# Performance work log

Hardware: AMD Instinct MI355X
Metric: run time of the kernel (lower is better)

The kernel has to match this reference:

```python
import jax, jax.numpy as jnp
import numpy as np

N_HEAD, D_MODEL, D_K, D_V, D_O = 16, 1024, 64, 64, 1024
B, S = 4, 2048


def setup_inputs() -> dict:
    key = jax.random.key(0)
    ks = jax.random.split(key, 11)
    s = 0.02
    return {
        "q": jax.random.normal(ks[0], (B, S, D_MODEL), jnp.float32),
        "k": jax.random.normal(ks[1], (B, S, D_MODEL), jnp.float32),
        "v": jax.random.normal(ks[2], (B, S, D_MODEL), jnp.float32),
        "Wq": jax.random.normal(ks[3], (D_MODEL, N_HEAD * D_K), jnp.float32) * s,
        "bq": jnp.zeros((N_HEAD * D_K,), jnp.float32),
        "Wk": jax.random.normal(ks[4], (D_MODEL, N_HEAD * D_K), jnp.float32) * s,
        "bk": jnp.zeros((N_HEAD * D_K,), jnp.float32),
        "Wv": jax.random.normal(ks[5], (D_MODEL, N_HEAD * D_V), jnp.float32) * s,
        "bv": jnp.zeros((N_HEAD * D_V,), jnp.float32),
        "Wo": jax.random.normal(ks[6], (N_HEAD * D_V, D_O), jnp.float32) * s,
        "bo": jnp.zeros((D_O,), jnp.float32),
    }


def reference(q, k, v, Wq, bq, Wk, bk, Wv, bv, Wo, bo):
    b, n_q, _ = q.shape
    # QKV projections -> [b, s, h, d]
    qh = (q @ Wq + bq).reshape(b, -1, N_HEAD, D_K)
    kh = (k @ Wk + bk).reshape(b, -1, N_HEAD, D_K)
    vh = (v @ Wv + bv).reshape(b, -1, N_HEAD, D_V)
    scale = jnp.asarray(np.power(D_K, 0.5), qh.dtype)
    # scores [b, h, n_q, n_k]
    scores = jnp.einsum("bqhd,bkhd->bhqk", qh, kh) / scale
    attn = jax.nn.softmax(scores, axis=-1)
    out = jnp.einsum("bhqk,bkhd->bqhd", attn, vh).reshape(b, n_q, N_HEAD * D_V)
    return out @ Wo + bo
```

## Files before the change

### kernel.cpp

```cpp
#include <hip/hip_runtime.h>
#include <hip/hip_bf16.h>


typedef __attribute__((ext_vector_type(8))) short bf16x8;
typedef __attribute__((ext_vector_type(4))) float f32x4;
typedef __attribute__((ext_vector_type(4))) unsigned short u16x4;

#define QSCALE 0.1803368801111244f

__device__ __forceinline__ unsigned short f2bf(float x) {
  unsigned u = __builtin_bit_cast(unsigned, x);
  u += 0x7fffu + ((u >> 16) & 1u);
  return (unsigned short)(u >> 16);
}

__device__ __forceinline__ short f2bf_s(float x) {
  __hip_bfloat16 h = __float2bfloat16(x);
  return __builtin_bit_cast(short, h);
}

__device__ __forceinline__ float fexp2(float x) {
#if __has_builtin(__builtin_amdgcn_exp2f)
  return __builtin_amdgcn_exp2f(x);
#else
  return exp2f(x);
#endif
}

__global__ void wtrans4(const float* __restrict__ W0, const float* __restrict__ W1,
                        const float* __restrict__ W2, const float* __restrict__ W3,
                        unsigned short* __restrict__ WT) {
  __shared__ float t[32][33];
  int x = threadIdx.x, y = threadIdx.y;
  int k0 = blockIdx.x * 32, n0 = blockIdx.y * 32;
  int z = blockIdx.z;
  const float* W = z == 0 ? W0 : z == 1 ? W1 : z == 2 ? W2 : W3;
  float scale = z == 0 ? QSCALE : 1.0f;
  unsigned short* dst = WT + (size_t)z * (1024 * 1024);
#pragma unroll
  for (int i = 0; i < 4; i++)
    t[y + i * 8][x] = W[(k0 + y + i * 8) * 1024 + n0 + x];
  __syncthreads();
#pragma unroll
  for (int i = 0; i < 4; i++)
    dst[(n0 + y + i * 8) * 1024 + k0 + x] = f2bf(t[x][y + i * 8] * scale);
}

template <bool AF32, int MODE>
__global__ __launch_bounds__(256, 2) void gemm128(
    const void* __restrict__ Ap, const unsigned short* __restrict__ BT,
    const float* __restrict__ bias, float bscale, void* __restrict__ Cp) {
  __shared__ __align__(16) char As[8192];
  __shared__ __align__(16) char Bs[8192];
  const int K = 1024;
  int tid = threadIdx.x;
  int lane = tid & 63;
  int w = tid >> 6;
  int wr = w >> 1, wc = w & 1;
  int bid = blockIdx.x;
  int sid = (bid & 7) * 64 + (bid >> 3);
  int m0 = (sid >> 3) * 128, n0 = (sid & 7) * 128;
  int r = tid >> 1;
  int kb = (tid & 1) << 4;

  f32x4 acc[4][4];
#pragma unroll
  for (int i = 0; i < 4; i++)
#pragma unroll
    for (int j = 0; j < 4; j++) acc[i][j] = (f32x4){0.f, 0.f, 0.f, 0.f};

  const float* Af = (const float*)Ap;
  const unsigned short* Ab = (const unsigned short*)Ap;

  f32x4 afr[4];
  bf16x8 afb[2];
  bf16x8 bfr[2];

  if (AF32) {
    const f32x4* p = (const f32x4*)(Af + (size_t)(m0 + r) * K + kb);
#pragma unroll
    for (int i = 0; i < 4; i++) afr[i] = p[i];
  } else {
    const bf16x8* p = (const bf16x8*)(Ab + (size_t)(m0 + r) * K + kb);
    afb[0] = p[0]; afb[1] = p[1];
  }
  {
    const bf16x8* p = (const bf16x8*)(BT + (size_t)(n0 + r) * K + kb);
    bfr[0] = p[0]; bfr[1] = p[1];
  }

  int swz = (r & 7) << 4;
  int wbyte = r * 64 + kb * 2;
  int cc = lane & 15, g = lane >> 4;

  for (int k0 = 0; k0 < K; k0 += 32) {
    __syncthreads();
    if (AF32) {
      bf16x8 s0, s1;
#pragma unroll
      for (int i = 0; i < 8; i++) {
        s0[i] = (short)f2bf(afr[i >> 2][i & 3]);
        s1[i] = (short)f2bf(afr[2 + (i >> 2)][i & 3]);
      }
      *(bf16x8*)(As + (wbyte ^ swz)) = s0;
      *(bf16x8*)(As + ((wbyte + 16) ^ swz)) = s1;
    } else {
      *(bf16x8*)(As + (wbyte ^ swz)) = afb[0];
      *(bf16x8*)(As + ((wbyte + 16) ^ swz)) = afb[1];
    }
    *(bf16x8*)(Bs + (wbyte ^ swz)) = bfr[0];
    *(bf16x8*)(Bs + ((wbyte + 16) ^ swz)) = bfr[1];
    if (k0 + 32 < K) {
      if (AF32) {
        const f32x4* p = (const f32x4*)(Af + (size_t)(m0 + r) * K + k0 + 32 + kb);
#pragma unroll
        for (int i = 0; i < 4; i++) afr[i] = p[i];
      } else {
        const bf16x8* p = (const bf16x8*)(Ab + (size_t)(m0 + r) * K + k0 + 32 + kb);
        afb[0] = p[0]; afb[1] = p[1];
      }
      const bf16x8* p = (const bf16x8*)(BT + (size_t)(n0 + r) * K + k0 + 32 + kb);
      bfr[0] = p[0]; bfr[1] = p[1];
    }
    __syncthreads();
    bf16x8 a[4], b[4];
#pragma unroll
    for (int mi = 0; mi < 4; mi++) {
      int row = wr * 64 + mi * 16 + cc;
      int byte = (row * 64 + g * 16) ^ ((row & 7) << 4);
      a[mi] = *(const bf16x8*)(As + byte);
    }
#pragma unroll
    for (int ni = 0; ni < 4; ni++) {
      int row = wc * 64 + ni * 16 + cc;
      int byte = (row * 64 + g * 16) ^ ((row & 7) << 4);
      b[ni] = *(const bf16x8*)(Bs + byte);
    }
#pragma unroll
    for (int mi = 0; mi < 4; mi++)
#pragma unroll
      for (int ni = 0; ni < 4; ni++)
        acc[mi][ni] =
            __builtin_amdgcn_mfma_f32_16x16x32_bf16(a[mi], b[ni], acc[mi][ni], 0, 0, 0);
  }

#pragma unroll
  for (int ni = 0; ni < 4; ni++) {
    int n = n0 + wc * 64 + ni * 16 + cc;
    float bv = bias[n] * bscale;
#pragma unroll
    for (int mi = 0; mi < 4; mi++) {
      int mbase = m0 + wr * 64 + mi * 16 + g * 4;
      if (MODE == 2) {
        u16x4 pk;
#pragma unroll
        for (int j = 0; j < 4; j++) pk[j] = f2bf(acc[mi][ni][j] + bv);
        int bb = mbase >> 11, s = mbase & 2047;
        int sp = (s & ~31) | ((((s & 15) >> 2) << 3) + (((s >> 4) & 1) << 2));
        int hh = n >> 6, d = n & 63;
        *(u16x4*)&((unsigned short*)Cp)[(((size_t)(bb * 16 + hh) * 64 + d) << 11) + sp] = pk;
      } else {
#pragma unroll
        for (int j = 0; j < 4; j++) {
          float val = acc[mi][ni][j] + bv;
          int m = mbase + j;
          if (MODE == 0) {
            int bb = m >> 11, s = m & 2047;
            int hh = n >> 6, d = n & 63;
            ((unsigned short*)Cp)[(((bb * 16 + hh) * 2048 + s) << 6) + d] = f2bf(val);
          } else {
            ((float*)Cp)[(size_t)m * 1024 + n] = val;
          }
        }
      }
    }
  }
}

__global__ __launch_bounds__(512, 2) void attn64(
    const unsigned short* __restrict__ Qh, const unsigned short* __restrict__ Kh,
    const unsigned short* __restrict__ Vt, unsigned short* __restrict__ O) {
  __shared__ __align__(16) char Ks[2][16384];
  __shared__ __align__(16) char Vs[2][16384];
  int tid = threadIdx.x, lane = tid & 63, w = tid >> 6;
  int bid = blockIdx.x;
  int sid = (bid & 7) * 64 + (bid >> 3);
  int bh = sid >> 3, qb = sid & 7;
  int b = bh >> 4, h = bh & 15;
  const unsigned short* Q  = Qh + (size_t)bh * (2048 * 64);
  const unsigned short* Kb = Kh + (size_t)bh * (2048 * 64);
  const unsigned short* Vb = Vt + (size_t)bh * (64 * 2048);
  int q0 = qb * 256 + w * 32;
  int cc = lane & 15, g = lane >> 4, g4 = g << 2;

  bf16x8 vones;
#pragma unroll
  for (int i = 0; i < 8; i++) vones[i] = (short)0x3F80;

  bf16x8 aq0[2], aq1[2];
#pragma unroll
  for (int g2 = 0; g2 < 2; g2++) {
    aq0[g2] = *(const bf16x8*)(Q + (size_t)(q0 + cc) * 64 + g2 * 32 + g * 8);
    aq1[g2] = *(const bf16x8*)(Q + (size_t)(q0 + 16 + cc) * 64 + g2 * 32 + g * 8);
  }

  f32x4 oacc0[4], oacc1[4];
#pragma unroll
  for (int df = 0; df < 4; df++) {
    oacc0[df] = (f32x4){0.f, 0.f, 0.f, 0.f};
    oacc1[df] = (f32x4){0.f, 0.f, 0.f, 0.f};
  }
  f32x4 lacc0 = (f32x4){0.f, 0.f, 0.f, 0.f};
  f32x4 lacc1 = (f32x4){0.f, 0.f, 0.f, 0.f};

  int kr = tid >> 2, kseg = tid & 3;
  int vr = tid >> 3, vq = tid & 7;
  int kswz = (kr & 7) << 4;
  int vswz = (vr & 7) << 4;
  int kbyte = kr * 128 + kseg * 32;
  int vbyte = vr * 256 + vq * 32;

  bf16x8 kv[2], vv[2];
  {
    const bf16x8* pK = (const bf16x8*)(Kb + (size_t)kr * 64 + kseg * 16);
    const bf16x8* pV = (const bf16x8*)(Vb + (size_t)vr * 2048 + vq * 16);
    kv[0] = pK[0]; kv[1] = pK[1];
    vv[0] = pV[0]; vv[1] = pV[1];
  }
#pragma unroll
  for (int i = 0; i < 2; i++) {
    *(bf16x8*)(Ks[0] + ((kbyte + i * 16) ^ kswz)) = kv[i];
    *(bf16x8*)(Vs[0] + ((vbyte + i * 16) ^ vswz)) = vv[i];
  }
  int cur = 0;

  for (int kt = 0; kt < 2048; kt += 128) {
    __syncthreads();
    if (kt + 128 < 2048) {
      const bf16x8* pK = (const bf16x8*)(Kb + (size_t)(kt + 128 + kr) * 64 + kseg * 16);
      const bf16x8* pV = (const bf16x8*)(Vb + (size_t)vr * 2048 + kt + 128 + vq * 16);
      kv[0] = pK[0]; kv[1] = pK[1];
      vv[0] = pV[0]; vv[1] = pV[1];
    }
    const char* Kc = Ks[cur];
    const char* Vc = Vs[cur];

    f32x4 sc0[8], sc1[8];
#pragma unroll
    for (int nf = 0; nf < 8; nf++) {
      sc0[nf] = (f32x4){0.f, 0.f, 0.f, 0.f};
      sc1[nf] = (f32x4){0.f, 0.f, 0.f, 0.f};
    }
    __builtin_amdgcn_s_setprio(1);
#pragma unroll
    for (int nf = 0; nf < 8; nf++) {
#pragma unroll
      for (int g2 = 0; g2 < 2; g2++) {
        int rk = nf * 16 + cc;
        int byte = (rk * 128 + g2 * 64 + g * 16) ^ ((rk & 7) << 4);
        bf16x8 bk = *(const bf16x8*)(Kc + byte);
        sc0[nf] = __builtin_amdgcn_mfma_f32_16x16x32_bf16(bk, aq0[g2], sc0[nf], 0, 0, 0);
        sc1[nf] = __builtin_amdgcn_mfma_f32_16x16x32_bf16(bk, aq1[g2], sc1[nf], 0, 0, 0);
      }
    }
    __builtin_amdgcn_s_setprio(0);

#pragma unroll
    for (int nf = 0; nf < 8; nf++)
#pragma unroll
      for (int t = 0; t < 4; t++) {
        sc0[nf][t] = fexp2(sc0[nf][t]);
        sc1[nf][t] = fexp2(sc1[nf][t]);
      }

    bf16x8 pa0[4], pa1[4];
#pragma unroll
    for (int kk = 0; kk < 4; kk++) {
#pragma unroll
      for (int i = 0; i < 4; i++) {
        pa0[kk][i]     = f2bf_s(sc0[2 * kk][i]);
        pa0[kk][4 + i] = f2bf_s(sc0[2 * kk + 1][i]);
        pa1[kk][i]     = f2bf_s(sc1[2 * kk][i]);
        pa1[kk][4 + i] = f2bf_s(sc1[2 * kk + 1][i]);
      }
    }
    __builtin_amdgcn_s_setprio(1);
#pragma unroll
    for (int df = 0; df < 4; df++) {
#pragma unroll
      for (int kk = 0; kk < 4; kk++) {
        int rv = df * 16 + cc;
        int byte = (rv * 256 + kk * 64 + g * 16) ^ ((rv & 7) << 4);
        bf16x8 bv = *(const bf16x8*)(Vc + byte);
        oacc0[df] = __builtin_amdgcn_mfma_f32_16x16x32_bf16(pa0[kk], bv, oacc0[df], 0, 0, 0);
        oacc1[df] = __builtin_amdgcn_mfma_f32_16x16x32_bf16(pa1[kk], bv, oacc1[df], 0, 0, 0);
      }
    }
#pragma unroll
    for (int kk = 0; kk < 4; kk++) {
      lacc0 = __builtin_amdgcn_mfma_f32_16x16x32_bf16(pa0[kk], vones, lacc0, 0, 0, 0);
      lacc1 = __builtin_amdgcn_mfma_f32_16x16x32_bf16(pa1[kk], vones, lacc1, 0, 0, 0);
    }
    __builtin_amdgcn_s_setprio(0);

    if (kt + 128 < 2048) {
      char* Kn = Ks[cur ^ 1];
      char* Vn = Vs[cur ^ 1];
#pragma unroll
      for (int i = 0; i < 2; i++) {
        *(bf16x8*)(Kn + ((kbyte + i * 16) ^ kswz)) = kv[i];
        *(bf16x8*)(Vn + ((vbyte + i * 16) ^ vswz)) = vv[i];
      }
    }
    cur ^= 1;
  }

#pragma unroll
  for (int t = 0; t < 4; t++) {
    float inv0 = 1.0f / lacc0[t];
    float inv1 = 1.0f / lacc1[t];
    int srow = q0 + g4 + t;
#pragma unroll
    for (int df = 0; df < 4; df++) {
      int d = df * 16 + cc;
      O[((size_t)b * 2048 + srow) * 1024 + h * 64 + d]        = f2bf(oacc0[df][t] * inv0);
      O[((size_t)b * 2048 + srow + 16) * 1024 + h * 64 + d]   = f2bf(oacc1[df][t] * inv1);
    }
  }
}

extern "C" void kernel_launch(void* const* d_in, const int* in_sizes, int n_in,
                              void* d_out, int out_size, void* d_ws, size_t ws_size,
                              hipStream_t stream) {
  const float* q  = (const float*)d_in[0];
  const float* k  = (const float*)d_in[1];
  const float* v  = (const float*)d_in[2];
  const float* Wq = (const float*)d_in[3];
  const float* bq = (const float*)d_in[4];
  const float* Wk = (const float*)d_in[5];
  const float* bk = (const float*)d_in[6];
  const float* Wv = (const float*)d_in[7];
  const float* bv = (const float*)d_in[8];
  const float* Wo = (const float*)d_in[9];
  const float* bo = (const float*)d_in[10];

  char* ws = (char*)d_ws;
  const size_t MB = 1024 * 1024;
  unsigned short* WqT = (unsigned short*)(ws + 0 * MB);
  unsigned short* WkT = (unsigned short*)(ws + 2 * MB);
  unsigned short* WvT = (unsigned short*)(ws + 4 * MB);
  unsigned short* WoT = (unsigned short*)(ws + 6 * MB);
  unsigned short* qh  = (unsigned short*)(ws + 8 * MB);
  unsigned short* kh  = (unsigned short*)(ws + 24 * MB);
  unsigned short* vt  = (unsigned short*)(ws + 40 * MB);
  unsigned short* ao  = (unsigned short*)(ws + 56 * MB);

  wtrans4<<<dim3(32, 32, 4), dim3(32, 8), 0, stream>>>(Wq, Wk, Wv, Wo, WqT);

  gemm128<true, 0><<<512, 256, 0, stream>>>(q, WqT, bq, QSCALE, qh);
  gemm128<true, 0><<<512, 256, 0, stream>>>(k, WkT, bk, 1.0f, kh);
  gemm128<true, 2><<<512, 256, 0, stream>>>(v, WvT, bv, 1.0f, vt);

  attn64<<<512, 512, 0, stream>>>(qh, kh, vt, ao);

  gemm128<false, 1><<<512, 256, 0, stream>>>(ao, WoT, bo, 1.0f, d_out);
}
```

Measured before the change: 204.7 us.

## Use direct global-to-LDS loads in GEMM and shrink attention blocks

The GEMM now loads the bf16 B tiles, and the A tile when it is already bf16, directly from global memory into LDS with global_load_lds. This drops the register staging and the extra LDS stores, and uses a new XOR swizzle that matches the load pattern. The attention kernel moves to 256-thread blocks with 128 queries each and 64-key tiles, with half the LDS per block and twice as many blocks, to raise occupancy. Risks: the direct loads are synchronised only by __syncthreads with a single buffer, so load latency may be exposed, and the smaller key tiles mean more barriers per key.

```diff
diff --git a/kernel.cpp b/kernel.cpp
--- a/kernel.cpp
+++ b/kernel.cpp
@@ -25,6 +25,12 @@
 #else
   return exp2f(x);
 #endif
+}
+
+__device__ __forceinline__ void gload16(const void* g, void* l) {
+  __builtin_amdgcn_global_load_lds(
+      (const __attribute__((address_space(1))) unsigned int*)g,
+      (__attribute__((address_space(3))) unsigned int*)l, 16, 0, 0);
 }
 
 __global__ void wtrans4(const float* __restrict__ W0, const float* __restrict__ W1,
@@ -60,8 +66,20 @@
   int bid = blockIdx.x;
   int sid = (bid & 7) * 64 + (bid >> 3);
   int m0 = (sid >> 3) * 128, n0 = (sid & 7) * 128;
+
+  int p0 = w * 2048 + lane * 16;
+  int p1 = p0 + 1024;
+  int row0 = p0 >> 6, col0 = (p0 & 63) ^ (((p0 >> 7) & 3) << 4);
+  int row1 = p1 >> 6, col1 = (p1 & 63) ^ (((p1 >> 7) & 3) << 4);
+  const char* srcB0 = (const char*)BT + (size_t)(n0 + row0) * 2048 + col0;
+  const char* srcB1 = (const char*)BT + (size_t)(n0 + row1) * 2048 + col1;
+  const char* srcA0 = (const char*)Ap + (size_t)(m0 + row0) * 2048 + col0;
+  const char* srcA1 = (const char*)Ap + (size_t)(m0 + row1) * 2048 + col1;
+
   int r = tid >> 1;
   int kb = (tid & 1) << 4;
+  int wbyte = r * 64 + (kb << 1);
+  int amask = ((r >> 1) & 3) << 4;
 
   f32x4 acc[4][4];
 #pragma unroll
@@ -70,27 +88,13 @@
     for (int j = 0; j < 4; j++) acc[i][j] = (f32x4){0.f, 0.f, 0.f, 0.f};
 
   const float* Af = (const float*)Ap;
-  const unsigned short* Ab = (const unsigned short*)Ap;
-
   f32x4 afr[4];
-  bf16x8 afb[2];
-  bf16x8 bfr[2];
-
   if (AF32) {
     const f32x4* p = (const f32x4*)(Af + (size_t)(m0 + r) * K + kb);
 #pragma unroll
     for (int i = 0; i < 4; i++) afr[i] = p[i];
-  } else {
-    const bf16x8* p = (const bf16x8*)(Ab + (size_t)(m0 + r) * K + kb);
-    afb[0] = p[0]; afb[1] = p[1];
-  }
-  {
-    const bf16x8* p = (const bf16x8*)(BT + (size_t)(n0 + r) * K + kb);
-    bfr[0] = p[0]; bfr[1] = p[1];
-  }
-
-  int swz = (r & 7) << 4;
-  int wbyte = r * 64 + kb * 2;
+  }
+
   int cc = lane & 15, g = lane >> 4;
 
   for (int k0 = 0; k0 < K; k0 += 32) {
@@ -102,39 +106,32 @@
         s0[i] = (short)f2bf(afr[i >> 2][i & 3]);
         s1[i] = (short)f2bf(afr[2 + (i >> 2)][i & 3]);
       }
-      *(bf16x8*)(As + (wbyte ^ swz)) = s0;
-      *(bf16x8*)(As + ((wbyte + 16) ^ swz)) = s1;
+      *(bf16x8*)(As + (wbyte ^ amask)) = s0;
+      *(bf16x8*)(As + ((wbyte + 16) ^ amask)) = s1;
     } else {
-      *(bf16x8*)(As + (wbyte ^ swz)) = afb[0];
-      *(bf16x8*)(As + ((wbyte + 16) ^ swz)) = afb[1];
-    }
-    *(bf16x8*)(Bs + (wbyte ^ swz)) = bfr[0];
-    *(bf16x8*)(Bs + ((wbyte + 16) ^ swz)) = bfr[1];
-    if (k0 + 32 < K) {
-      if (AF32) {
-        const f32x4* p = (const f32x4*)(Af + (size_t)(m0 + r) * K + k0 + 32 + kb);
-#pragma unroll
-        for (int i = 0; i < 4; i++) afr[i] = p[i];
-      } else {
-        const bf16x8* p = (const bf16x8*)(Ab + (size_t)(m0 + r) * K + k0 + 32 + kb);
-        afb[0] = p[0]; afb[1] = p[1];
-      }
-      const bf16x8* p = (const bf16x8*)(BT + (size_t)(n0 + r) * K + k0 + 32 + kb);
-      bfr[0] = p[0]; bfr[1] = p[1];
-    }
+      gload16(srcA0 + k0 * 2, As + w * 2048);
+      gload16(srcA1 + k0 * 2, As + w * 2048 + 1024);
+    }
+    gload16(srcB0 + k0 * 2, Bs + w * 2048);
+    gload16(srcB1 + k0 * 2, Bs + w * 2048 + 1024);
     __syncthreads();
+    if (AF32 && k0 + 32 < K) {
+      const f32x4* p = (const f32x4*)(Af + (size_t)(m0 + r) * K + k0 + 32 + kb);
+#pragma unroll
+      for (int i = 0; i < 4; i++) afr[i] = p[i];
+    }
     bf16x8 a[4], b[4];
 #pragma unroll
     for (int mi = 0; mi < 4; mi++) {
       int row = wr * 64 + mi * 16 + cc;
-      int byte = (row * 64 + g * 16) ^ ((row & 7) << 4);
-      a[mi] = *(const bf16x8*)(As + byte);
+      int x = row * 64 + g * 16;
+      a[mi] = *(const bf16x8*)(As + (x ^ (((row >> 1) & 3) << 4)));
     }
 #pragma unroll
     for (int ni = 0; ni < 4; ni++) {
       int row = wc * 64 + ni * 16 + cc;
-      int byte = (row * 64 + g * 16) ^ ((row & 7) << 4);
-      b[ni] = *(const bf16x8*)(Bs + byte);
+      int x = row * 64 + g * 16;
+      b[ni] = *(const bf16x8*)(Bs + (x ^ (((row >> 1) & 3) << 4)));
     }
 #pragma unroll
     for (int mi = 0; mi < 4; mi++)
@@ -177,20 +174,20 @@
   }
 }
 
-__global__ __launch_bounds__(512, 2) void attn64(
+__global__ __launch_bounds__(256, 4) void attn64(
     const unsigned short* __restrict__ Qh, const unsigned short* __restrict__ Kh,
     const unsigned short* __restrict__ Vt, unsigned short* __restrict__ O) {
-  __shared__ __align__(16) char Ks[2][16384];
-  __shared__ __align__(16) char Vs[2][16384];
+  __shared__ __align__(16) char Ks[2][8192];
+  __shared__ __align__(16) char Vs[2][8192];
   int tid = threadIdx.x, lane = tid & 63, w = tid >> 6;
   int bid = blockIdx.x;
-  int sid = (bid & 7) * 64 + (bid >> 3);
-  int bh = sid >> 3, qb = sid & 7;
+  int sid = (bid & 7) * 128 + (bid >> 3);
+  int bh = sid >> 4, qb = sid & 15;
   int b = bh >> 4, h = bh & 15;
   const unsigned short* Q  = Qh + (size_t)bh * (2048 * 64);
   const unsigned short* Kb = Kh + (size_t)bh * (2048 * 64);
   const unsigned short* Vb = Vt + (size_t)bh * (64 * 2048);
-  int q0 = qb * 256 + w * 32;
+  int q0 = qb * 128 + w * 32;
   int cc = lane & 15, g = lane >> 4, g4 = g << 2;
 
   bf16x8 vones;
@@ -213,47 +210,44 @@
   f32x4 lacc0 = (f32x4){0.f, 0.f, 0.f, 0.f};
   f32x4 lacc1 = (f32x4){0.f, 0.f, 0.f, 0.f};
 
-  int kr = tid >> 2, kseg = tid & 3;
-  int vr = tid >> 3, vq = tid & 7;
+  int kr = tid >> 2, kq = tid & 3;
   int kswz = (kr & 7) << 4;
-  int vswz = (vr & 7) << 4;
-  int kbyte = kr * 128 + kseg * 32;
-  int vbyte = vr * 256 + vq * 32;
+  int kbyte = kr * 128 + kq * 32;
 
   bf16x8 kv[2], vv[2];
   {
-    const bf16x8* pK = (const bf16x8*)(Kb + (size_t)kr * 64 + kseg * 16);
-    const bf16x8* pV = (const bf16x8*)(Vb + (size_t)vr * 2048 + vq * 16);
+    const bf16x8* pK = (const bf16x8*)(Kb + (size_t)kr * 64 + kq * 16);
+    const bf16x8* pV = (const bf16x8*)(Vb + (size_t)kr * 2048 + kq * 16);
     kv[0] = pK[0]; kv[1] = pK[1];
     vv[0] = pV[0]; vv[1] = pV[1];
   }
 #pragma unroll
   for (int i = 0; i < 2; i++) {
     *(bf16x8*)(Ks[0] + ((kbyte + i * 16) ^ kswz)) = kv[i];
-    *(bf16x8*)(Vs[0] + ((vbyte + i * 16) ^ vswz)) = vv[i];
+    *(bf16x8*)(Vs[0] + ((kbyte + i * 16) ^ kswz)) = vv[i];
   }
   int cur = 0;
 
-  for (int kt = 0; kt < 2048; kt += 128) {
+  for (int kt = 0; kt < 2048; kt += 64) {
     __syncthreads();
-    if (kt + 128 < 2048) {
-      const bf16x8* pK = (const bf16x8*)(Kb + (size_t)(kt + 128 + kr) * 64 + kseg * 16);
-      const bf16x8* pV = (const bf16x8*)(Vb + (size_t)vr * 2048 + kt + 128 + vq * 16);
+    if (kt + 64 < 2048) {
+      const bf16x8* pK = (const bf16x8*)(Kb + (size_t)(kt + 64 + kr) * 64 + kq * 16);
+      const bf16x8* pV = (const bf16x8*)(Vb + (size_t)kr * 2048 + kt + 64 + kq * 16);
       kv[0] = pK[0]; kv[1] = pK[1];
       vv[0] = pV[0]; vv[1] = pV[1];
     }
     const char* Kc = Ks[cur];
     const char* Vc = Vs[cur];
 
-    f32x4 sc0[8], sc1[8];
-#pragma unroll
-    for (int nf = 0; nf < 8; nf++) {
+    f32x4 sc0[4], sc1[4];
+#pragma unroll
+    for (int nf = 0; nf < 4; nf++) {
       sc0[nf] = (f32x4){0.f, 0.f, 0.f, 0.f};
       sc1[nf] = (f32x4){0.f, 0.f, 0.f, 0.f};
     }
     __builtin_amdgcn_s_setprio(1);
 #pragma unroll
-    for (int nf = 0; nf < 8; nf++) {
+    for (int nf = 0; nf < 4; nf++) {
 #pragma unroll
       for (int g2 = 0; g2 < 2; g2++) {
         int rk = nf * 16 + cc;
@@ -266,16 +260,16 @@
     __builtin_amdgcn_s_setprio(0);
 
 #pragma unroll
-    for (int nf = 0; nf < 8; nf++)
+    for (int nf = 0; nf < 4; nf++)
 #pragma unroll
       for (int t = 0; t < 4; t++) {
         sc0[nf][t] = fexp2(sc0[nf][t]);
         sc1[nf][t] = fexp2(sc1[nf][t]);
       }
 
-    bf16x8 pa0[4], pa1[4];
-#pragma unroll
-    for (int kk = 0; kk < 4; kk++) {
+    bf16x8 pa0[2], pa1[2];
+#pragma unroll
+    for (int kk = 0; kk < 2; kk++) {
 #pragma unroll
       for (int i = 0; i < 4; i++) {
         pa0[kk][i]     = f2bf_s(sc0[2 * kk][i]);
@@ -288,28 +282,28 @@
 #pragma unroll
     for (int df = 0; df < 4; df++) {
 #pragma unroll
-      for (int kk = 0; kk < 4; kk++) {
+      for (int kk = 0; kk < 2; kk++) {
         int rv = df * 16 + cc;
-        int byte = (rv * 256 + kk * 64 + g * 16) ^ ((rv & 7) << 4);
+        int byte = (rv * 128 + kk * 64 + g * 16) ^ ((rv & 7) << 4);
         bf16x8 bv = *(const bf16x8*)(Vc + byte);
         oacc0[df] = __builtin_amdgcn_mfma_f32_16x16x32_bf16(pa0[kk], bv, oacc0[df], 0, 0, 0);
         oacc1[df] = __builtin_amdgcn_mfma_f32_16x16x32_bf16(pa1[kk], bv, oacc1[df], 0, 0, 0);
       }
     }
 #pragma unroll
-    for (int kk = 0; kk < 4; kk++) {
+    for (int kk = 0; kk < 2; kk++) {
       lacc0 = __builtin_amdgcn_mfma_f32_16x16x32_bf16(pa0[kk], vones, lacc0, 0, 0, 0);
       lacc1 = __builtin_amdgcn_mfma_f32_16x16x32_bf16(pa1[kk], vones, lacc1, 0, 0, 0);
     }
     __builtin_amdgcn_s_setprio(0);
 
-    if (kt + 128 < 2048) {
+    if (kt + 64 < 2048) {
       char* Kn = Ks[cur ^ 1];
       char* Vn = Vs[cur ^ 1];
 #pragma unroll
       for (int i = 0; i < 2; i++) {
         *(bf16x8*)(Kn + ((kbyte + i * 16) ^ kswz)) = kv[i];
-        *(bf16x8*)(Vn + ((vbyte + i * 16) ^ vswz)) = vv[i];
+        *(bf16x8*)(Vn + ((kbyte + i * 16) ^ kswz)) = vv[i];
       }
     }
     cur ^= 1;
@@ -323,8 +317,8 @@
 #pragma unroll
     for (int df = 0; df < 4; df++) {
       int d = df * 16 + cc;
-      O[((size_t)b * 2048 + srow) * 1024 + h * 64 + d]        = f2bf(oacc0[df][t] * inv0);
-      O[((size_t)b * 2048 + srow + 16) * 1024 + h * 64 + d]   = f2bf(oacc1[df][t] * inv1);
+      O[((size_t)b * 2048 + srow) * 1024 + h * 64 + d]      = f2bf(oacc0[df][t] * inv0);
+      O[((size_t)b * 2048 + srow + 16) * 1024 + h * 64 + d] = f2bf(oacc1[df][t] * inv1);
     }
   }
 }
@@ -361,7 +355,7 @@
   gemm128<true, 0><<<512, 256, 0, stream>>>(k, WkT, bk, 1.0f, kh);
   gemm128<true, 2><<<512, 256, 0, stream>>>(v, WvT, bv, 1.0f, vt);
 
-  attn64<<<512, 512, 0, stream>>>(qh, kh, vt, ao);
+  attn64<<<1024, 256, 0, stream>>>(qh, kh, vt, ao);
 
   gemm128<false, 1><<<512, 256, 0, stream>>>(ao, WoT, bo, 1.0f, d_out);
 }
```

After: 224.9 us. 9.9% more time.
